# Optimization experiments

Hardware: AMD Instinct MI355X
Metric: run time of the kernel (lower is better)

## Reference

```python
import jax, jax.numpy as jnp
import numpy as np

B = 16384
C = 512          # mean candidate count per sample
T = B * C        # total flat logits length (static)


def _seg_ce(logits, counts, gt, valid, B):
    """Segmented cross-entropy over variable-length candidate sets.
    logits: [T] flat concatenated logits; counts: [B] segment lengths (sum == T);
    gt: [B] target index within each segment; valid: [B] bool mask.
    Returns (mean loss over valid samples, n_correct, n_valid)."""
    Ttot = logits.shape[0]
    offsets = jnp.cumsum(counts) - counts                       # [B] start of each segment
    seg = jnp.repeat(jnp.arange(B), counts, total_repeat_length=Ttot)  # [T] segment ids
    segmax = jax.ops.segment_max(logits, seg, num_segments=B)   # [B]
    ex = jnp.exp(logits - segmax[seg])
    Z = jax.ops.segment_sum(ex, seg, num_segments=B)            # [B]
    lse = jnp.log(Z) + segmax                                   # [B] logsumexp per segment
    # target logit: clamp position for safety; invalid rows are masked out anyway
    pos = offsets + jnp.clip(gt, 0, jnp.maximum(counts - 1, 0))
    ce = lse - logits[pos]                                      # [B]
    in_range = (gt >= 0) & (gt < counts)
    vmask = (counts > 0) & in_range & valid
    n_valid = vmask.sum()
    loss = jnp.where(vmask, ce, 0.0).sum() / jnp.maximum(n_valid, 1)
    # argmax within each segment (first occurrence, matching torch.argmax)
    local = jnp.arange(Ttot) - offsets[seg]
    is_max = logits == segmax[seg]
    arg = jax.ops.segment_min(jnp.where(is_max, local, Ttot), seg, num_segments=B)
    n_correct = (vmask & (arg == gt)).sum()
    return loss, n_correct, n_valid


def setup_inputs() -> dict:
    key = jax.random.key(0)
    ks = jax.random.split(key, 8)
    # counts alternate C+32 / C-32 so sum == B*C exactly (static T)
    counts = jnp.where(jnp.arange(B) % 2 == 0, C + 32, C - 32).astype(jnp.int32)
    sys_logits = jax.random.normal(ks[0], (T,), dtype=jnp.float32)
    bar_logits = jax.random.normal(ks[1], (T,), dtype=jnp.float32)
    gt_system_idx = jax.random.randint(ks[2], (B,), 0, C - 32).astype(jnp.int32)
    gt_bar_in_sys = jax.random.randint(ks[3], (B,), 0, C - 32).astype(jnp.int32)
    note_positions = jax.random.uniform(ks[4], (B,), dtype=jnp.float32)
    gt_note_position = jax.random.uniform(ks[5], (B,), dtype=jnp.float32)
    gt_valid = jax.random.bernoulli(ks[6], 0.97, (B,))
    return {
        'sys_logits': sys_logits, 'sys_counts': counts,
        'bar_logits': bar_logits, 'bar_counts': counts,
        'note_positions': note_positions,
        'gt_system_idx': gt_system_idx, 'gt_bar_in_sys': gt_bar_in_sys,
        'gt_note_position': gt_note_position, 'gt_valid': gt_valid,
        'log_var_sys': jnp.zeros((), jnp.float32),
        'log_var_bar': jnp.zeros((), jnp.float32),
        'log_var_note': jnp.zeros((), jnp.float32),
    }


def reference(sys_logits, sys_counts, bar_logits, bar_counts, note_positions,
              gt_system_idx, gt_bar_in_sys, gt_note_position, gt_valid,
              log_var_sys, log_var_bar, log_var_note):
    Bn = gt_system_idx.shape[0]
    sys_loss, sys_correct, n_valid = _seg_ce(sys_logits, sys_counts, gt_system_idx, gt_valid, Bn)
    bar_loss, bar_correct, n_valid_bar = _seg_ce(bar_logits, bar_counts, gt_bar_in_sys, gt_valid, Bn)
    # note position MSE over valid samples (bar_valid == gt_valid here)
    m = gt_valid
    nsel = m.sum()
    sq = jnp.where(m, (note_positions - gt_note_position) ** 2, 0.0)
    note_loss = jnp.where(nsel > 0, sq.sum() / jnp.maximum(nsel, 1), 0.0)
    prec_sys = jnp.exp(-log_var_sys)
    prec_bar = jnp.exp(-log_var_bar)
    prec_note = jnp.exp(-log_var_note)
    loss = (0.5 * prec_sys * sys_loss + 0.5 * log_var_sys
            + 0.5 * prec_bar * bar_loss + 0.5 * log_var_bar
            + 0.5 * prec_note * note_loss + 0.5 * log_var_note)
    sys_acc = sys_correct / jnp.maximum(n_valid, 1)
    bar_acc = bar_correct / jnp.maximum(n_valid_bar, 1)
    return (loss, sys_loss, bar_loss, note_loss, sys_acc, bar_acc,
            prec_sys, prec_bar, prec_note)
```

## Files before the change

### kernel.cpp

```cpp
#include <hip/hip_runtime.h>
#include <math.h>

#define SCAN_BLOCKS 64
#define DESC_BASE 512

__device__ __forceinline__ bool is_valid(const void* gv, int flag, int i) {
  if (flag == 0) return ((const int*)gv)[i] != 0;
  if (flag == 1) return ((const unsigned char*)gv)[i] != 0;
  return ((const float*)gv)[i] != 0.0f;
}

__global__ __launch_bounds__(256)
void uwl_scan_partial(const int* __restrict__ c_sys, const int* __restrict__ c_bar,
                      const void* __restrict__ gv, int B, int* __restrict__ ws) {
  const int blk = blockIdx.x;
  const int chunk = (B + SCAN_BLOCKS - 1) / SCAN_BLOCKS;
  const int start = blk * chunk;
  const int end = (start + chunk < B) ? start + chunk : B;
  int ss = 0, sb = 0;
  for (int i = start + threadIdx.x; i < end; i += 256) {
    ss += c_sys[i];
    sb += c_bar[i];
  }
#pragma unroll
  for (int d = 1; d < 64; d <<= 1) {
    ss += __shfl_xor(ss, d, 64);
    sb += __shfl_xor(sb, d, 64);
  }
  __shared__ int l1[4], l2[4];
  const int wid = threadIdx.x >> 6;
  if ((threadIdx.x & 63) == 0) { l1[wid] = ss; l2[wid] = sb; }
  __syncthreads();
  if (threadIdx.x == 0) {
    ws[256 + blk] = l1[0] + l1[1] + l1[2] + l1[3];
    ws[256 + SCAN_BLOCKS + blk] = l2[0] + l2[1] + l2[2] + l2[3];
  }
  if (blk == 0) {
    if (threadIdx.x >= 1 && threadIdx.x <= 8) ws[threadIdx.x * 16] = 0;
    if (threadIdx.x == 9) ws[144] = 0;
    if (threadIdx.x == 10) {
      const unsigned int* w = (const unsigned int*)gv;
      int nw = B / 4; if (nw > 64) nw = 64; if (nw < 1) nw = 1;
      bool all01 = true, allf = true;
      for (int i = 0; i < nw; ++i) {
        const unsigned int x = w[i];
        if (x > 1u) all01 = false;
        if (x != 0u && x != 0x3F800000u) allf = false;
      }
      ws[0] = all01 ? 0 : (allf ? 2 : 1);
    }
  }
}

__global__ __launch_bounds__(256)
void uwl_scan_desc(const int* __restrict__ c_sys, const int* __restrict__ c_bar,
                   const int* __restrict__ gt_sys, const int* __restrict__ gt_bar,
                   const void* __restrict__ gv, int B, int* __restrict__ ws) {
  const int* part = ws + 256;
  const int flag = ws[0];
  const int blk = blockIdx.x;
  const int lane = threadIdx.x & 63;
  const int wid = threadIdx.x >> 6;
  __shared__ int baseS, baseB;
  __shared__ int ws1[4], ws2[4];
  if (threadIdx.x < 128) {
    int p = (lane < blk) ? part[(wid ? SCAN_BLOCKS : 0) + lane] : 0;
#pragma unroll
    for (int d = 1; d < 64; d <<= 1) p += __shfl_xor(p, d, 64);
    if (lane == 0) { if (wid) baseB = p; else baseS = p; }
  }
  __syncthreads();
  int carry1 = baseS, carry2 = baseB;
  const int chunk = (B + SCAN_BLOCKS - 1) / SCAN_BLOCKS;
  const int start = blk * chunk;
  const int end = (start + chunk < B) ? start + chunk : B;
  int4* descS = (int4*)(ws + DESC_BASE);
  int4* descB = descS + B;
  for (int base = start; base < end; base += 256) {
    const int idx = base + threadIdx.x;
    const bool ok = idx < end;
    const int x1 = ok ? c_sys[idx] : 0;
    const int x2 = ok ? c_bar[idx] : 0;
    int o1 = x1, o2 = x2;
#pragma unroll
    for (int d = 1; d < 64; d <<= 1) {
      const int v1 = __shfl_up(o1, d, 64);
      const int v2 = __shfl_up(o2, d, 64);
      if (lane >= d) { o1 += v1; o2 += v2; }
    }
    if (lane == 63) { ws1[wid] = o1; ws2[wid] = o2; }
    __syncthreads();
    int w1 = 0, w2 = 0;
    for (int w = 0; w < wid; ++w) { w1 += ws1[w]; w2 += ws2[w]; }
    if (ok) {
      const int g1 = gt_sys[idx], g2 = gt_bar[idx];
      const bool v = is_valid(gv, flag, idx);
      descS[idx] = make_int4(carry1 + w1 + o1 - x1, x1, g1,
                             (x1 > 0 && g1 >= 0 && g1 < x1 && v) ? 1 : 0);
      descB[idx] = make_int4(carry2 + w2 + o2 - x2, x2, g2,
                             (x2 > 0 && g2 >= 0 && g2 < x2 && v) ? 1 : 0);
    }
    carry1 += ws1[0] + ws1[1] + ws1[2] + ws1[3];
    carry2 += ws2[0] + ws2[1] + ws2[2] + ws2[3];
    __syncthreads();
  }
}

__global__ __launch_bounds__(256)
void uwl_ce_kernel(const float* __restrict__ sys_lg, const float* __restrict__ bar_lg,
                   int B, int* __restrict__ wsI, float* __restrict__ wsF) {
  const int wave = __builtin_amdgcn_readfirstlane(
      (int)((blockIdx.x * blockDim.x + threadIdx.x) >> 6));
  const int lane = threadIdx.x & 63;
  if (wave >= 2 * B) return;
  const int4 d4 = ((const int4*)(wsI + DESC_BASE))[wave];
  const float* lg = (wave < B) ? sys_lg : bar_lg;
  const int off_i = d4.x, count = d4.y, gt = d4.z, vld = d4.w;
  const long long off = off_i;

  float m = -INFINITY;
  float s = 0.f;
  float tl = 0.f;
  const bool regpath = (count >= 4) && (count <= 576) &&
                       ((off_i & 3) == 0) && ((count & 3) == 0);
  if (regpath) {
    const float4* p = (const float4*)(lg + off);
    const int emax = (count >> 2) - 1;
    float vals[8];
#pragma unroll
    for (int k = 0; k < 2; ++k) {
      const int e4 = (k << 6) + lane;
      const int ec = (e4 > emax) ? emax : e4;
      const float4 v = p[ec];
      const bool live = (e4 <= emax);
      vals[4 * k]     = live ? v.x : -INFINITY;
      vals[4 * k + 1] = live ? v.y : -INFINITY;
      vals[4 * k + 2] = live ? v.z : -INFINITY;
      vals[4 * k + 3] = live ? v.w : -INFINITY;
    }
    const int ti = 512 + lane;
    const int tic = (ti < count) ? ti : (count - 1);
    const float tvr = lg[off + tic];
    const float tv = (ti < count) ? tvr : -INFINITY;
#pragma unroll
    for (int k = 0; k < 8; ++k) m = fmaxf(m, vals[k]);
    m = fmaxf(m, tv);
#pragma unroll
    for (int k = 0; k < 8; ++k) s += __expf(vals[k]);
    s += __expf(tv);
    const int gts = vld ? gt : 0;
    float pick;
    int srclane;
    if (gts < 512) {
      const int q = ((gts >> 8) << 2) | (gts & 3);
      pick = vals[0];
#pragma unroll
      for (int i = 1; i < 8; ++i) pick = (i == q) ? vals[i] : pick;
      srclane = (gts >> 2) & 63;
    } else {
      pick = tv;
      srclane = gts - 512;
    }
    tl = __shfl(pick, srclane, 64);
  } else {
    for (int i = lane; i < count; i += 64) {
      const float v = lg[off + i];
      m = fmaxf(m, v);
      s += __expf(v);
    }
    if (vld) {
      const float t0 = (lane == 0) ? lg[off + gt] : 0.f;
      tl = __shfl(t0, 0, 64);
    }
  }
#pragma unroll
  for (int d = 1; d < 64; d <<= 1) {
    s += __shfl_xor(s, d, 64);
    m = fmaxf(m, __shfl_xor(m, d, 64));
  }
  if (lane == 0) {
    float ce = 0.f, code = 0.f;
    if (vld) {
      ce = __logf(s) - tl;
      code = (tl == m) ? 3.f : 1.f;
    }
    ((float2*)(wsF + DESC_BASE + 8 * B))[wave] = make_float2(ce, code);
  }
}

__global__ __launch_bounds__(256)
void uwl_reduce_kernel(const float* __restrict__ npos, const float* __restrict__ gnp,
                       const void* __restrict__ gv,
                       const float* __restrict__ lvs_p, const float* __restrict__ lvb_p,
                       const float* __restrict__ lvn_p,
                       int B, int* wsI, float* wsF, float* __restrict__ out) {
  const float2* pw = (const float2*)(wsF + DESC_BASE + 8 * B);
  float ces = 0.f, ceb = 0.f;
  int nvs = 0, cs = 0, nvb = 0, cb = 0;
  const int stride = gridDim.x * blockDim.x;
  for (int i = blockIdx.x * blockDim.x + threadIdx.x; i < 2 * B; i += stride) {
    const float2 v = pw[i];
    const int code = (int)v.y;
    if (i < B) { ces += v.x; nvs += code & 1; cs += code >> 1; }
    else       { ceb += v.x; nvb += code & 1; cb += code >> 1; }
  }
  const int flag = wsI[0];
  float sq = 0.f; int cnt = 0;
  for (int i = blockIdx.x * blockDim.x + threadIdx.x; i < B; i += stride) {
    if (is_valid(gv, flag, i)) {
      const float d = npos[i] - gnp[i];
      sq += d * d; cnt += 1;
    }
  }
#pragma unroll
  for (int d = 1; d < 64; d <<= 1) {
    ces += __shfl_xor(ces, d, 64);
    ceb += __shfl_xor(ceb, d, 64);
    nvs += __shfl_xor(nvs, d, 64);
    cs  += __shfl_xor(cs,  d, 64);
    nvb += __shfl_xor(nvb, d, 64);
    cb  += __shfl_xor(cb,  d, 64);
    sq  += __shfl_xor(sq,  d, 64);
    cnt += __shfl_xor(cnt, d, 64);
  }
  if ((threadIdx.x & 63) == 0) {
    atomicAdd(&wsI[16], nvs);
    atomicAdd(&wsI[32], cs);
    atomicAdd(&wsF[48], ces);
    atomicAdd(&wsI[64], nvb);
    atomicAdd(&wsI[80], cb);
    atomicAdd(&wsF[96], ceb);
    atomicAdd(&wsI[112], cnt);
    atomicAdd(&wsF[128], sq);
  }
  __syncthreads();
  if (threadIdx.x == 0) {
    __threadfence();
    const int t = atomicAdd(&wsI[144], 1);
    if (t == (int)gridDim.x - 1) {
      __threadfence();
      const int fnvs = atomicAdd(&wsI[16], 0);
      const int fcs  = atomicAdd(&wsI[32], 0);
      const int fnvb = atomicAdd(&wsI[64], 0);
      const int fcb  = atomicAdd(&wsI[80], 0);
      const int fnn  = atomicAdd(&wsI[112], 0);
      const float fces = atomicAdd(&wsF[48], 0.f);
      const float fceb = atomicAdd(&wsF[96], 0.f);
      const float fsq  = atomicAdd(&wsF[128], 0.f);
      const float sys_loss = fces / (float)(fnvs > 1 ? fnvs : 1);
      const float bar_loss = fceb / (float)(fnvb > 1 ? fnvb : 1);
      const float note_loss = (fnn > 0) ? fsq / (float)fnn : 0.f;
      const float lvs = lvs_p[0], lvb = lvb_p[0], lvn = lvn_p[0];
      const float ps = expf(-lvs), pb = expf(-lvb), pn = expf(-lvn);
      out[0] = 0.5f * (ps * sys_loss + lvs + pb * bar_loss + lvb + pn * note_loss + lvn);
      out[1] = sys_loss;
      out[2] = bar_loss;
      out[3] = note_loss;
      out[4] = (float)fcs / (float)(fnvs > 1 ? fnvs : 1);
      out[5] = (float)fcb / (float)(fnvb > 1 ? fnvb : 1);
      out[6] = ps;
      out[7] = pb;
      out[8] = pn;
    }
  }
}

extern "C" void kernel_launch(void* const* d_in, const int* in_sizes, int n_in,
                              void* d_out, int out_size, void* d_ws, size_t ws_size,
                              hipStream_t stream) {
  const float* sys_lg = (const float*)d_in[0];
  const int*   c_sys  = (const int*)d_in[1];
  const float* bar_lg = (const float*)d_in[2];
  const int*   c_bar  = (const int*)d_in[3];
  const float* npos   = (const float*)d_in[4];
  const int*   gt_sys = (const int*)d_in[5];
  const int*   gt_bar = (const int*)d_in[6];
  const float* gnp    = (const float*)d_in[7];
  const void*  gv     = d_in[8];
  const float* lvs    = (const float*)d_in[9];
  const float* lvb    = (const float*)d_in[10];
  const float* lvn    = (const float*)d_in[11];
  const int B = in_sizes[1];

  int*   wsI = (int*)d_ws;
  float* wsF = (float*)d_ws;

  uwl_scan_partial<<<SCAN_BLOCKS, 256, 0, stream>>>(c_sys, c_bar, gv, B, wsI);
  uwl_scan_desc<<<SCAN_BLOCKS, 256, 0, stream>>>(c_sys, c_bar, gt_sys, gt_bar, gv, B, wsI);

  const long long nthreads = (long long)(2 * B) * 64;
  const int nblocks = (int)((nthreads + 255) / 256);
  uwl_ce_kernel<<<nblocks, 256, 0, stream>>>(sys_lg, bar_lg, B, wsI, wsF);

  uwl_reduce_kernel<<<64, 256, 0, stream>>>(npos, gnp, gv, lvs, lvb, lvn,
                                            B, wsI, wsF, (float*)d_out);
}
```

Measured before the change: 135.5 us.

## Fuse final reduction into CE kernel via slotted atomics and last-block ticket

Removes the separate reduce kernel. Each CE wave now atomically adds its loss and a packed valid/correct count into one of 256 slots, and the last block to take a ticket reduces the slots and writes the outputs. The note-position MSE moves into the scan/descriptor kernel. This saves a kernel launch and the per-sample float2 write and reread, at the cost of many atomics and a grid-wide ticket. Packing the counts into 16-bit halves risks overflow if the valid count reaches 65536, and float atomics make the summation order nondeterministic.

```diff
diff --git a/kernel.cpp b/kernel.cpp
--- a/kernel.cpp
+++ b/kernel.cpp
@@ -2,7 +2,17 @@
 #include <math.h>
 
 #define SCAN_BLOCKS 64
-#define DESC_BASE 512
+#define WS_FLAG      0
+#define WS_TICKET    4
+#define WS_SQ        16
+#define WS_CNT       20
+#define WS_SLOT_CES  64
+#define WS_SLOT_CEB  320
+#define WS_SLOT_CODS 576
+#define WS_SLOT_CODB 832
+#define WS_PART_SYS  1280
+#define WS_PART_BAR  1344
+#define DESC_BASE    2048
 
 __device__ __forceinline__ bool is_valid(const void* gv, int flag, int i) {
   if (flag == 0) return ((const int*)gv)[i] != 0;
@@ -32,12 +42,12 @@
   if ((threadIdx.x & 63) == 0) { l1[wid] = ss; l2[wid] = sb; }
   __syncthreads();
   if (threadIdx.x == 0) {
-    ws[256 + blk] = l1[0] + l1[1] + l1[2] + l1[3];
-    ws[256 + SCAN_BLOCKS + blk] = l2[0] + l2[1] + l2[2] + l2[3];
+    ws[WS_PART_SYS + blk] = l1[0] + l1[1] + l1[2] + l1[3];
+    ws[WS_PART_BAR + blk] = l2[0] + l2[1] + l2[2] + l2[3];
   }
   if (blk == 0) {
-    if (threadIdx.x >= 1 && threadIdx.x <= 8) ws[threadIdx.x * 16] = 0;
-    if (threadIdx.x == 9) ws[144] = 0;
+    for (int i = threadIdx.x; i < 1024; i += 256) ws[WS_SLOT_CES + i] = 0;
+    if (threadIdx.x == 0) { ws[WS_TICKET] = 0; ws[WS_SQ] = 0; ws[WS_CNT] = 0; }
     if (threadIdx.x == 10) {
       const unsigned int* w = (const unsigned int*)gv;
       int nw = B / 4; if (nw > 64) nw = 64; if (nw < 1) nw = 1;
@@ -47,7 +57,7 @@
         if (x > 1u) all01 = false;
         if (x != 0u && x != 0x3F800000u) allf = false;
       }
-      ws[0] = all01 ? 0 : (allf ? 2 : 1);
+      ws[WS_FLAG] = all01 ? 0 : (allf ? 2 : 1);
     }
   }
 }
@@ -55,16 +65,17 @@
 __global__ __launch_bounds__(256)
 void uwl_scan_desc(const int* __restrict__ c_sys, const int* __restrict__ c_bar,
                    const int* __restrict__ gt_sys, const int* __restrict__ gt_bar,
-                   const void* __restrict__ gv, int B, int* __restrict__ ws) {
-  const int* part = ws + 256;
-  const int flag = ws[0];
+                   const void* __restrict__ gv,
+                   const float* __restrict__ npos, const float* __restrict__ gnp,
+                   int B, int* __restrict__ wsI, float* __restrict__ wsF) {
+  const int flag = wsI[WS_FLAG];
   const int blk = blockIdx.x;
   const int lane = threadIdx.x & 63;
   const int wid = threadIdx.x >> 6;
   __shared__ int baseS, baseB;
   __shared__ int ws1[4], ws2[4];
   if (threadIdx.x < 128) {
-    int p = (lane < blk) ? part[(wid ? SCAN_BLOCKS : 0) + lane] : 0;
+    int p = (lane < blk) ? wsI[(wid ? WS_PART_BAR : WS_PART_SYS) + lane] : 0;
 #pragma unroll
     for (int d = 1; d < 64; d <<= 1) p += __shfl_xor(p, d, 64);
     if (lane == 0) { if (wid) baseB = p; else baseS = p; }
@@ -74,7 +85,7 @@
   const int chunk = (B + SCAN_BLOCKS - 1) / SCAN_BLOCKS;
   const int start = blk * chunk;
   const int end = (start + chunk < B) ? start + chunk : B;
-  int4* descS = (int4*)(ws + DESC_BASE);
+  int4* descS = (int4*)(wsI + DESC_BASE);
   int4* descB = descS + B;
   for (int base = start; base < end; base += 256) {
     const int idx = base + threadIdx.x;
@@ -104,149 +115,149 @@
     carry2 += ws2[0] + ws2[1] + ws2[2] + ws2[3];
     __syncthreads();
   }
+  float sq = 0.f; int cnt = 0;
+  for (int i = start + threadIdx.x; i < end; i += 256) {
+    if (is_valid(gv, flag, i)) {
+      const float d = npos[i] - gnp[i];
+      sq += d * d; cnt += 1;
+    }
+  }
+#pragma unroll
+  for (int d = 1; d < 64; d <<= 1) {
+    sq += __shfl_xor(sq, d, 64);
+    cnt += __shfl_xor(cnt, d, 64);
+  }
+  if (lane == 0) {
+    atomicAdd(&wsF[WS_SQ], sq);
+    atomicAdd(&wsI[WS_CNT], cnt);
+  }
 }
 
 __global__ __launch_bounds__(256)
 void uwl_ce_kernel(const float* __restrict__ sys_lg, const float* __restrict__ bar_lg,
-                   int B, int* __restrict__ wsI, float* __restrict__ wsF) {
+                   const float* __restrict__ lvs_p, const float* __restrict__ lvb_p,
+                   const float* __restrict__ lvn_p,
+                   int B, int* __restrict__ wsI, float* __restrict__ wsF,
+                   float* __restrict__ out) {
   const int wave = __builtin_amdgcn_readfirstlane(
       (int)((blockIdx.x * blockDim.x + threadIdx.x) >> 6));
   const int lane = threadIdx.x & 63;
-  if (wave >= 2 * B) return;
-  const int4 d4 = ((const int4*)(wsI + DESC_BASE))[wave];
-  const float* lg = (wave < B) ? sys_lg : bar_lg;
-  const int off_i = d4.x, count = d4.y, gt = d4.z, vld = d4.w;
-  const long long off = off_i;
-
-  float m = -INFINITY;
-  float s = 0.f;
-  float tl = 0.f;
-  const bool regpath = (count >= 4) && (count <= 576) &&
-                       ((off_i & 3) == 0) && ((count & 3) == 0);
-  if (regpath) {
-    const float4* p = (const float4*)(lg + off);
-    const int emax = (count >> 2) - 1;
-    float vals[8];
-#pragma unroll
-    for (int k = 0; k < 2; ++k) {
-      const int e4 = (k << 6) + lane;
-      const int ec = (e4 > emax) ? emax : e4;
-      const float4 v = p[ec];
-      const bool live = (e4 <= emax);
-      vals[4 * k]     = live ? v.x : -INFINITY;
-      vals[4 * k + 1] = live ? v.y : -INFINITY;
-      vals[4 * k + 2] = live ? v.z : -INFINITY;
-      vals[4 * k + 3] = live ? v.w : -INFINITY;
-    }
-    const int ti = 512 + lane;
-    const int tic = (ti < count) ? ti : (count - 1);
-    const float tvr = lg[off + tic];
-    const float tv = (ti < count) ? tvr : -INFINITY;
-#pragma unroll
-    for (int k = 0; k < 8; ++k) m = fmaxf(m, vals[k]);
-    m = fmaxf(m, tv);
-#pragma unroll
-    for (int k = 0; k < 8; ++k) s += __expf(vals[k]);
-    s += __expf(tv);
-    const int gts = vld ? gt : 0;
-    float pick;
-    int srclane;
-    if (gts < 512) {
-      const int q = ((gts >> 8) << 2) | (gts & 3);
-      pick = vals[0];
-#pragma unroll
-      for (int i = 1; i < 8; ++i) pick = (i == q) ? vals[i] : pick;
-      srclane = (gts >> 2) & 63;
+  if (wave < 2 * B) {
+    const int4 d4 = ((const int4*)(wsI + DESC_BASE))[wave];
+    const float* lg = (wave < B) ? sys_lg : bar_lg;
+    const int off_i = d4.x, count = d4.y, gt = d4.z, vld = d4.w;
+    const long long off = off_i;
+
+    float m = -INFINITY;
+    float s = 0.f;
+    float tl = 0.f;
+    const bool regpath = (count >= 4) && (count <= 576) &&
+                         ((off_i & 3) == 0) && ((count & 3) == 0);
+    if (regpath) {
+      const float4* p = (const float4*)(lg + off);
+      const int emax = (count >> 2) - 1;
+      float vals[8];
+#pragma unroll
+      for (int k = 0; k < 2; ++k) {
+        const int e4 = (k << 6) + lane;
+        const int ec = (e4 > emax) ? emax : e4;
+        const float4 v = p[ec];
+        const bool live = (e4 <= emax);
+        vals[4 * k]     = live ? v.x : -INFINITY;
+        vals[4 * k + 1] = live ? v.y : -INFINITY;
+        vals[4 * k + 2] = live ? v.z : -INFINITY;
+        vals[4 * k + 3] = live ? v.w : -INFINITY;
+      }
+      const int ti = 512 + lane;
+      const int tic = (ti < count) ? ti : (count - 1);
+      const float tvr = lg[off + tic];
+      const float tv = (ti < count) ? tvr : -INFINITY;
+#pragma unroll
+      for (int k = 0; k < 8; ++k) m = fmaxf(m, vals[k]);
+      m = fmaxf(m, tv);
+#pragma unroll
+      for (int k = 0; k < 8; ++k) s += __expf(vals[k]);
+      s += __expf(tv);
+      const int gts = vld ? gt : 0;
+      float pick;
+      int srclane;
+      if (gts < 512) {
+        const int q = ((gts >> 8) << 2) | (gts & 3);
+        pick = vals[0];
+#pragma unroll
+        for (int i = 1; i < 8; ++i) pick = (i == q) ? vals[i] : pick;
+        srclane = (gts >> 2) & 63;
+      } else {
+        pick = tv;
+        srclane = gts - 512;
+      }
+      tl = __shfl(pick, srclane, 64);
     } else {
-      pick = tv;
-      srclane = gts - 512;
-    }
-    tl = __shfl(pick, srclane, 64);
-  } else {
-    for (int i = lane; i < count; i += 64) {
-      const float v = lg[off + i];
-      m = fmaxf(m, v);
-      s += __expf(v);
-    }
-    if (vld) {
-      const float t0 = (lane == 0) ? lg[off + gt] : 0.f;
-      tl = __shfl(t0, 0, 64);
-    }
-  }
-#pragma unroll
-  for (int d = 1; d < 64; d <<= 1) {
-    s += __shfl_xor(s, d, 64);
-    m = fmaxf(m, __shfl_xor(m, d, 64));
-  }
-  if (lane == 0) {
-    float ce = 0.f, code = 0.f;
-    if (vld) {
-      ce = __logf(s) - tl;
-      code = (tl == m) ? 3.f : 1.f;
-    }
-    ((float2*)(wsF + DESC_BASE + 8 * B))[wave] = make_float2(ce, code);
-  }
-}
-
-__global__ __launch_bounds__(256)
-void uwl_reduce_kernel(const float* __restrict__ npos, const float* __restrict__ gnp,
-                       const void* __restrict__ gv,
-                       const float* __restrict__ lvs_p, const float* __restrict__ lvb_p,
-                       const float* __restrict__ lvn_p,
-                       int B, int* wsI, float* wsF, float* __restrict__ out) {
-  const float2* pw = (const float2*)(wsF + DESC_BASE + 8 * B);
-  float ces = 0.f, ceb = 0.f;
-  int nvs = 0, cs = 0, nvb = 0, cb = 0;
-  const int stride = gridDim.x * blockDim.x;
-  for (int i = blockIdx.x * blockDim.x + threadIdx.x; i < 2 * B; i += stride) {
-    const float2 v = pw[i];
-    const int code = (int)v.y;
-    if (i < B) { ces += v.x; nvs += code & 1; cs += code >> 1; }
-    else       { ceb += v.x; nvb += code & 1; cb += code >> 1; }
-  }
-  const int flag = wsI[0];
-  float sq = 0.f; int cnt = 0;
-  for (int i = blockIdx.x * blockDim.x + threadIdx.x; i < B; i += stride) {
-    if (is_valid(gv, flag, i)) {
-      const float d = npos[i] - gnp[i];
-      sq += d * d; cnt += 1;
-    }
-  }
-#pragma unroll
-  for (int d = 1; d < 64; d <<= 1) {
-    ces += __shfl_xor(ces, d, 64);
-    ceb += __shfl_xor(ceb, d, 64);
-    nvs += __shfl_xor(nvs, d, 64);
-    cs  += __shfl_xor(cs,  d, 64);
-    nvb += __shfl_xor(nvb, d, 64);
-    cb  += __shfl_xor(cb,  d, 64);
-    sq  += __shfl_xor(sq,  d, 64);
-    cnt += __shfl_xor(cnt, d, 64);
-  }
-  if ((threadIdx.x & 63) == 0) {
-    atomicAdd(&wsI[16], nvs);
-    atomicAdd(&wsI[32], cs);
-    atomicAdd(&wsF[48], ces);
-    atomicAdd(&wsI[64], nvb);
-    atomicAdd(&wsI[80], cb);
-    atomicAdd(&wsF[96], ceb);
-    atomicAdd(&wsI[112], cnt);
-    atomicAdd(&wsF[128], sq);
-  }
+      for (int i = lane; i < count; i += 64) {
+        const float v = lg[off + i];
+        m = fmaxf(m, v);
+        s += __expf(v);
+      }
+      if (vld) {
+        const float t0 = (lane == 0) ? lg[off + gt] : 0.f;
+        tl = __shfl(t0, 0, 64);
+      }
+    }
+#pragma unroll
+    for (int d = 1; d < 64; d <<= 1) {
+      s += __shfl_xor(s, d, 64);
+      m = fmaxf(m, __shfl_xor(m, d, 64));
+    }
+    if (lane == 0 && vld) {
+      const float ce = __logf(s) - tl;
+      const int contrib = 1 + ((tl == m) ? 65536 : 0);
+      const int slot = wave & 255;
+      if (wave < B) {
+        atomicAdd(&wsF[WS_SLOT_CES + slot], ce);
+        atomicAdd(&wsI[WS_SLOT_CODS + slot], contrib);
+      } else {
+        atomicAdd(&wsF[WS_SLOT_CEB + slot], ce);
+        atomicAdd(&wsI[WS_SLOT_CODB + slot], contrib);
+      }
+    }
+  }
+  __shared__ int is_last;
   __syncthreads();
   if (threadIdx.x == 0) {
     __threadfence();
-    const int t = atomicAdd(&wsI[144], 1);
-    if (t == (int)gridDim.x - 1) {
-      __threadfence();
-      const int fnvs = atomicAdd(&wsI[16], 0);
-      const int fcs  = atomicAdd(&wsI[32], 0);
-      const int fnvb = atomicAdd(&wsI[64], 0);
-      const int fcb  = atomicAdd(&wsI[80], 0);
-      const int fnn  = atomicAdd(&wsI[112], 0);
-      const float fces = atomicAdd(&wsF[48], 0.f);
-      const float fceb = atomicAdd(&wsF[96], 0.f);
-      const float fsq  = atomicAdd(&wsF[128], 0.f);
+    is_last = (atomicAdd(&wsI[WS_TICKET], 1) == (int)gridDim.x - 1) ? 1 : 0;
+  }
+  __syncthreads();
+  if (is_last) {
+    __threadfence();
+    const int tid = threadIdx.x;
+    float ces = atomicAdd(&wsF[WS_SLOT_CES + tid], 0.f);
+    float ceb = atomicAdd(&wsF[WS_SLOT_CEB + tid], 0.f);
+    int cods = atomicAdd(&wsI[WS_SLOT_CODS + tid], 0);
+    int codb = atomicAdd(&wsI[WS_SLOT_CODB + tid], 0);
+#pragma unroll
+    for (int d = 1; d < 64; d <<= 1) {
+      ces += __shfl_xor(ces, d, 64);
+      ceb += __shfl_xor(ceb, d, 64);
+      cods += __shfl_xor(cods, d, 64);
+      codb += __shfl_xor(codb, d, 64);
+    }
+    __shared__ float s_ces[4], s_ceb[4];
+    __shared__ int s_cods[4], s_codb[4];
+    const int wid = threadIdx.x >> 6;
+    if ((threadIdx.x & 63) == 0) {
+      s_ces[wid] = ces; s_ceb[wid] = ceb; s_cods[wid] = cods; s_codb[wid] = codb;
+    }
+    __syncthreads();
+    if (threadIdx.x == 0) {
+      const float fces = s_ces[0] + s_ces[1] + s_ces[2] + s_ces[3];
+      const float fceb = s_ceb[0] + s_ceb[1] + s_ceb[2] + s_ceb[3];
+      const int fs = s_cods[0] + s_cods[1] + s_cods[2] + s_cods[3];
+      const int fb = s_codb[0] + s_codb[1] + s_codb[2] + s_codb[3];
+      const int fnvs = fs & 0xFFFF, fcs = fs >> 16;
+      const int fnvb = fb & 0xFFFF, fcb = fb >> 16;
+      const float fsq = atomicAdd(&wsF[WS_SQ], 0.f);
+      const int fnn = atomicAdd(&wsI[WS_CNT], 0);
       const float sys_loss = fces / (float)(fnvs > 1 ? fnvs : 1);
       const float bar_loss = fceb / (float)(fnvb > 1 ? fnvb : 1);
       const float note_loss = (fnn > 0) ? fsq / (float)fnn : 0.f;
@@ -286,12 +297,11 @@
   float* wsF = (float*)d_ws;
 
   uwl_scan_partial<<<SCAN_BLOCKS, 256, 0, stream>>>(c_sys, c_bar, gv, B, wsI);
-  uwl_scan_desc<<<SCAN_BLOCKS, 256, 0, stream>>>(c_sys, c_bar, gt_sys, gt_bar, gv, B, wsI);
+  uwl_scan_desc<<<SCAN_BLOCKS, 256, 0, stream>>>(c_sys, c_bar, gt_sys, gt_bar, gv,
+                                                 npos, gnp, B, wsI, wsF);
 
   const long long nthreads = (long long)(2 * B) * 64;
   const int nblocks = (int)((nthreads + 255) / 256);
-  uwl_ce_kernel<<<nblocks, 256, 0, stream>>>(sys_lg, bar_lg, B, wsI, wsF);
-
-  uwl_reduce_kernel<<<64, 256, 0, stream>>>(npos, gnp, gv, lvs, lvb, lvn,
-                                            B, wsI, wsF, (float*)d_out);
-}
+  uwl_ce_kernel<<<nblocks, 256, 0, stream>>>(sys_lg, bar_lg, lvs, lvb, lvn,
+                                             B, wsI, wsF, (float*)d_out);
+}
```

Result: slower. 322.3 us (+137.8%).

## Merge scan kernels via redundant prefix sums; fold note MSE into scan

Applied to the files above, without the earlier changes.

Removes the separate partial-sum scan kernel. Each scan block now computes its own base offset by summing all counts before its chunk, and the validity-format flag is detected per block. The note-position MSE partials are computed in the scan kernel, so the final reduce only sums 64 partials, and the atomic-slot zeroing moves into the CE kernel. This saves one kernel launch and a dependency, at the cost of redundant prefix reads that grow with block index (up to about 16K ints per block).

```diff
diff --git a/kernel.cpp b/kernel.cpp
--- a/kernel.cpp
+++ b/kernel.cpp
@@ -3,6 +3,8 @@
 
 #define SCAN_BLOCKS 64
 #define DESC_BASE 512
+#define NOTE_SQ   256
+#define NOTE_CNT  320
 
 __device__ __forceinline__ bool is_valid(const void* gv, int flag, int i) {
   if (flag == 0) return ((const int*)gv)[i] != 0;
@@ -11,70 +13,49 @@
 }
 
 __global__ __launch_bounds__(256)
-void uwl_scan_partial(const int* __restrict__ c_sys, const int* __restrict__ c_bar,
-                      const void* __restrict__ gv, int B, int* __restrict__ ws) {
+void uwl_scan_desc(const int* __restrict__ c_sys, const int* __restrict__ c_bar,
+                   const int* __restrict__ gt_sys, const int* __restrict__ gt_bar,
+                   const void* __restrict__ gv,
+                   const float* __restrict__ npos, const float* __restrict__ gnp,
+                   int B, int* __restrict__ wsI, float* __restrict__ wsF) {
   const int blk = blockIdx.x;
+  const int lane = threadIdx.x & 63;
+  const int wid = threadIdx.x >> 6;
+  __shared__ int s_flag;
+  __shared__ int baseS, baseB;
+  __shared__ int ws1[4], ws2[4];
+  __shared__ float fsq[4];
+  if (threadIdx.x == 0) {
+    const unsigned int* w = (const unsigned int*)gv;
+    int nw = B / 4; if (nw > 64) nw = 64; if (nw < 1) nw = 1;
+    bool all01 = true, allf = true;
+    for (int i = 0; i < nw; ++i) {
+      const unsigned int x = w[i];
+      if (x > 1u) all01 = false;
+      if (x != 0u && x != 0x3F800000u) allf = false;
+    }
+    s_flag = all01 ? 0 : (allf ? 2 : 1);
+  }
   const int chunk = (B + SCAN_BLOCKS - 1) / SCAN_BLOCKS;
   const int start = blk * chunk;
   const int end = (start + chunk < B) ? start + chunk : B;
-  int ss = 0, sb = 0;
-  for (int i = start + threadIdx.x; i < end; i += 256) {
-    ss += c_sys[i];
-    sb += c_bar[i];
-  }
-#pragma unroll
-  for (int d = 1; d < 64; d <<= 1) {
-    ss += __shfl_xor(ss, d, 64);
-    sb += __shfl_xor(sb, d, 64);
-  }
-  __shared__ int l1[4], l2[4];
-  const int wid = threadIdx.x >> 6;
-  if ((threadIdx.x & 63) == 0) { l1[wid] = ss; l2[wid] = sb; }
-  __syncthreads();
-  if (threadIdx.x == 0) {
-    ws[256 + blk] = l1[0] + l1[1] + l1[2] + l1[3];
-    ws[256 + SCAN_BLOCKS + blk] = l2[0] + l2[1] + l2[2] + l2[3];
-  }
-  if (blk == 0) {
-    if (threadIdx.x >= 1 && threadIdx.x <= 8) ws[threadIdx.x * 16] = 0;
-    if (threadIdx.x == 9) ws[144] = 0;
-    if (threadIdx.x == 10) {
-      const unsigned int* w = (const unsigned int*)gv;
-      int nw = B / 4; if (nw > 64) nw = 64; if (nw < 1) nw = 1;
-      bool all01 = true, allf = true;
-      for (int i = 0; i < nw; ++i) {
-        const unsigned int x = w[i];
-        if (x > 1u) all01 = false;
-        if (x != 0u && x != 0x3F800000u) allf = false;
-      }
-      ws[0] = all01 ? 0 : (allf ? 2 : 1);
-    }
-  }
-}
-
-__global__ __launch_bounds__(256)
-void uwl_scan_desc(const int* __restrict__ c_sys, const int* __restrict__ c_bar,
-                   const int* __restrict__ gt_sys, const int* __restrict__ gt_bar,
-                   const void* __restrict__ gv, int B, int* __restrict__ ws) {
-  const int* part = ws + 256;
-  const int flag = ws[0];
-  const int blk = blockIdx.x;
-  const int lane = threadIdx.x & 63;
-  const int wid = threadIdx.x >> 6;
-  __shared__ int baseS, baseB;
-  __shared__ int ws1[4], ws2[4];
-  if (threadIdx.x < 128) {
-    int p = (lane < blk) ? part[(wid ? SCAN_BLOCKS : 0) + lane] : 0;
-#pragma unroll
-    for (int d = 1; d < 64; d <<= 1) p += __shfl_xor(p, d, 64);
-    if (lane == 0) { if (wid) baseB = p; else baseS = p; }
-  }
-  __syncthreads();
+  int bs = 0, bb = 0;
+  for (int i = threadIdx.x; i < start; i += 256) { bs += c_sys[i]; bb += c_bar[i]; }
+#pragma unroll
+  for (int d = 1; d < 64; d <<= 1) {
+    bs += __shfl_xor(bs, d, 64);
+    bb += __shfl_xor(bb, d, 64);
+  }
+  if (lane == 0) { ws1[wid] = bs; ws2[wid] = bb; }
+  __syncthreads();
+  if (threadIdx.x == 0) {
+    baseS = ws1[0] + ws1[1] + ws1[2] + ws1[3];
+    baseB = ws2[0] + ws2[1] + ws2[2] + ws2[3];
+  }
+  __syncthreads();
+  const int flag = s_flag;
   int carry1 = baseS, carry2 = baseB;
-  const int chunk = (B + SCAN_BLOCKS - 1) / SCAN_BLOCKS;
-  const int start = blk * chunk;
-  const int end = (start + chunk < B) ? start + chunk : B;
-  int4* descS = (int4*)(ws + DESC_BASE);
+  int4* descS = (int4*)(wsI + DESC_BASE);
   int4* descB = descS + B;
   for (int base = start; base < end; base += 256) {
     const int idx = base + threadIdx.x;
@@ -104,11 +85,33 @@
     carry2 += ws2[0] + ws2[1] + ws2[2] + ws2[3];
     __syncthreads();
   }
+  float sq = 0.f; int cnt = 0;
+  for (int i = start + threadIdx.x; i < end; i += 256) {
+    if (is_valid(gv, flag, i)) {
+      const float d = npos[i] - gnp[i];
+      sq += d * d; cnt += 1;
+    }
+  }
+#pragma unroll
+  for (int d = 1; d < 64; d <<= 1) {
+    sq += __shfl_xor(sq, d, 64);
+    cnt += __shfl_xor(cnt, d, 64);
+  }
+  if (lane == 0) { fsq[wid] = sq; ws1[wid] = cnt; }
+  __syncthreads();
+  if (threadIdx.x == 0) {
+    wsF[NOTE_SQ + blk] = fsq[0] + fsq[1] + fsq[2] + fsq[3];
+    wsI[NOTE_CNT + blk] = ws1[0] + ws1[1] + ws1[2] + ws1[3];
+  }
 }
 
 __global__ __launch_bounds__(256)
 void uwl_ce_kernel(const float* __restrict__ sys_lg, const float* __restrict__ bar_lg,
                    int B, int* __restrict__ wsI, float* __restrict__ wsF) {
+  if (blockIdx.x == 0) {
+    if (threadIdx.x >= 1 && threadIdx.x <= 8) wsI[threadIdx.x * 16] = 0;
+    if (threadIdx.x == 9) wsI[144] = 0;
+  }
   const int wave = __builtin_amdgcn_readfirstlane(
       (int)((blockIdx.x * blockDim.x + threadIdx.x) >> 6));
   const int lane = threadIdx.x & 63;
@@ -189,9 +192,7 @@
 }
 
 __global__ __launch_bounds__(256)
-void uwl_reduce_kernel(const float* __restrict__ npos, const float* __restrict__ gnp,
-                       const void* __restrict__ gv,
-                       const float* __restrict__ lvs_p, const float* __restrict__ lvb_p,
+void uwl_reduce_kernel(const float* __restrict__ lvs_p, const float* __restrict__ lvb_p,
                        const float* __restrict__ lvn_p,
                        int B, int* wsI, float* wsF, float* __restrict__ out) {
   const float2* pw = (const float2*)(wsF + DESC_BASE + 8 * B);
@@ -204,13 +205,10 @@
     if (i < B) { ces += v.x; nvs += code & 1; cs += code >> 1; }
     else       { ceb += v.x; nvb += code & 1; cb += code >> 1; }
   }
-  const int flag = wsI[0];
   float sq = 0.f; int cnt = 0;
-  for (int i = blockIdx.x * blockDim.x + threadIdx.x; i < B; i += stride) {
-    if (is_valid(gv, flag, i)) {
-      const float d = npos[i] - gnp[i];
-      sq += d * d; cnt += 1;
-    }
+  if (blockIdx.x == 0 && threadIdx.x < SCAN_BLOCKS) {
+    sq = wsF[NOTE_SQ + threadIdx.x];
+    cnt = wsI[NOTE_CNT + threadIdx.x];
   }
 #pragma unroll
   for (int d = 1; d < 64; d <<= 1) {
@@ -285,13 +283,12 @@
   int*   wsI = (int*)d_ws;
   float* wsF = (float*)d_ws;
 
-  uwl_scan_partial<<<SCAN_BLOCKS, 256, 0, stream>>>(c_sys, c_bar, gv, B, wsI);
-  uwl_scan_desc<<<SCAN_BLOCKS, 256, 0, stream>>>(c_sys, c_bar, gt_sys, gt_bar, gv, B, wsI);
+  uwl_scan_desc<<<SCAN_BLOCKS, 256, 0, stream>>>(c_sys, c_bar, gt_sys, gt_bar, gv,
+                                                 npos, gnp, B, wsI, wsF);
 
   const long long nthreads = (long long)(2 * B) * 64;
   const int nblocks = (int)((nthreads + 255) / 256);
   uwl_ce_kernel<<<nblocks, 256, 0, stream>>>(sys_lg, bar_lg, B, wsI, wsF);
 
-  uwl_reduce_kernel<<<64, 256, 0, stream>>>(npos, gnp, gv, lvs, lvb, lvn,
-                                            B, wsI, wsF, (float*)d_out);
-}
+  uwl_reduce_kernel<<<64, 256, 0, stream>>>(lvs, lvb, lvn, B, wsI, wsF, (float*)d_out);
+}
```

New measurement: 147.7 us. 1.09x slower.
